# Kernel optimization log

Hardware: AMD Instinct MI355X
Metric: run time of the kernel (lower is better)

The kernel has to match this reference:

```python
import jax, jax.numpy as jnp
import numpy as np

EPS = 1e-07

def setup_inputs() -> dict:
    key = jax.random.key(0)
    k1, k2, k3, k4 = jax.random.split(key, 4)
    B, IN, OUT = 8192, 2048, 2048
    input_tensor = jax.random.normal(k1, (B, IN), dtype=jnp.float32)
    # truncated_normal(stddev=0.02) init approximated with scaled normal
    W_hat = 0.02 * jax.random.normal(k2, (IN, OUT), dtype=jnp.float32)
    M_hat = 0.02 * jax.random.normal(k3, (IN, OUT), dtype=jnp.float32)
    gate = 0.02 * jax.random.normal(k4, (IN, OUT), dtype=jnp.float32)
    return {"input_tensor": input_tensor, "W_hat": W_hat, "M_hat": M_hat, "gate": gate}

def reference(input_tensor, W_hat, M_hat, gate):
    W = jnp.tanh(W_hat) * jax.nn.sigmoid(M_hat)          # [IN, OUT]
    a = input_tensor @ W                                  # additive path [B, OUT]
    m = jnp.exp(jnp.log(jnp.abs(input_tensor) + EPS) @ W) # multiplicative path [B, OUT]
    g = jax.nn.sigmoid(input_tensor @ gate)               # gate [B, OUT]
    return g * a + (1.0 - g) * m
```

## Files before the change

### kernel.cpp

```cpp
#include <hip/hip_runtime.h>
#include <stdint.h>

typedef __attribute__((ext_vector_type(8))) short short8;
typedef __attribute__((ext_vector_type(4))) float floatx4;

#define B_DIM 8192
#define K_DIM 2048
#define N_DIM 2048

__device__ __forceinline__ unsigned short f2bf(float f) {
    union { float f; unsigned u; } v; v.f = f;
    unsigned r = v.u + 0x7fffu + ((v.u >> 16) & 1u);
    return (unsigned short)(r >> 16);
}

__device__ __forceinline__ void gld_lds16(const void* g, void* l) {
    __builtin_amdgcn_global_load_lds(
        (const __attribute__((address_space(1))) void*)g,
        (__attribute__((address_space(3))) void*)l, 16, 0, 0);
}

__global__ __launch_bounds__(256) void prep_x(const float4* __restrict__ X4,
                                              ushort* __restrict__ Xb,
                                              ushort* __restrict__ Lb) {
    int i = blockIdx.x * 256 + threadIdx.x;
    float4 v = X4[i];
    ushort4 xb, lb;
    xb.x = f2bf(v.x); xb.y = f2bf(v.y); xb.z = f2bf(v.z); xb.w = f2bf(v.w);
    lb.x = f2bf(__logf(fabsf(v.x) + 1e-7f));
    lb.y = f2bf(__logf(fabsf(v.y) + 1e-7f));
    lb.z = f2bf(__logf(fabsf(v.z) + 1e-7f));
    lb.w = f2bf(__logf(fabsf(v.w) + 1e-7f));
    *(ushort4*)(Xb + (size_t)i * 4) = xb;
    *(ushort4*)(Lb + (size_t)i * 4) = lb;
}

__global__ __launch_bounds__(256) void prep_wg(const float* __restrict__ Wh,
                                               const float* __restrict__ Mh,
                                               const float* __restrict__ Gf,
                                               ushort* __restrict__ Wt,
                                               ushort* __restrict__ Gt) {
    __shared__ float tw[32][33];
    __shared__ float tg[32][33];
    const int k0 = blockIdx.y * 32, n0 = blockIdx.x * 32;
    const int tx = threadIdx.x, ty = threadIdx.y;
#pragma unroll
    for (int i = 0; i < 4; i++) {
        int k = k0 + ty + i * 8;
        int n = n0 + tx;
        size_t idx = (size_t)k * N_DIM + n;
        float wh = Wh[idx], mh = Mh[idx];
        tw[ty + i * 8][tx] = tanhf(wh) * (1.f / (1.f + __expf(-mh)));
        tg[ty + i * 8][tx] = Gf[idx];
    }
    __syncthreads();
#pragma unroll
    for (int i = 0; i < 4; i++) {
        int n = n0 + ty + i * 8;
        int k = k0 + tx;
        Wt[(size_t)n * K_DIM + k] = f2bf(tw[tx][ty + i * 8]);
        Gt[(size_t)n * K_DIM + k] = f2bf(tg[tx][ty + i * 8]);
    }
}

__global__ __launch_bounds__(256, 2) void gemm_fused(const ushort* __restrict__ Xb,
                                                     const ushort* __restrict__ Lb,
                                                     const ushort* __restrict__ Wt,
                                                     const ushort* __restrict__ Gt,
                                                     float* __restrict__ out) {
    __shared__ ushort smem[4 * 128 * 32];
    ushort* sX = smem;
    ushort* sL = smem + 1 * 128 * 32;
    ushort* sW = smem + 2 * 128 * 32;
    ushort* sG = smem + 3 * 128 * 32;

    const int t = threadIdx.x;
    const int lane = t & 63;
    const int w = t >> 6;
    const int wm = w >> 1, wn = w & 1;
    const int rowA = blockIdx.y * 128;
    const int rowB = blockIdx.x * 128;

    floatx4 acca[4][4], accm[4][4], accg[4][4];
    const floatx4 z = {0.f, 0.f, 0.f, 0.f};
#pragma unroll
    for (int i = 0; i < 4; i++)
#pragma unroll
        for (int j = 0; j < 4; j++) { acca[i][j] = z; accm[i][j] = z; accg[i][j] = z; }

    const int r0 = t >> 2;
    const int c8 = (t & 3) << 3;
    const int aoff0 = (rowA + r0) * K_DIM + c8;
    const int aoff1 = aoff0 + 64 * K_DIM;
    const int boff0 = (rowB + r0) * K_DIM + c8;
    const int boff1 = boff0 + 64 * K_DIM;

    const int lr = lane & 15;
    const int lk = (lane >> 4) << 3;
    const ushort* rdA = sX + (wm * 64 + lr) * 32 + lk;
    const ushort* rdB = sW + (wn * 64 + lr) * 32 + lk;

    for (int k0 = 0; k0 < K_DIM; k0 += 32) {
        gld_lds16(Xb + aoff0 + k0, sX + t * 8);
        gld_lds16(Xb + aoff1 + k0, sX + (t + 256) * 8);
        gld_lds16(Lb + aoff0 + k0, sL + t * 8);
        gld_lds16(Lb + aoff1 + k0, sL + (t + 256) * 8);
        gld_lds16(Wt + boff0 + k0, sW + t * 8);
        gld_lds16(Wt + boff1 + k0, sW + (t + 256) * 8);
        gld_lds16(Gt + boff0 + k0, sG + t * 8);
        gld_lds16(Gt + boff1 + k0, sG + (t + 256) * 8);
        asm volatile("s_waitcnt vmcnt(0)" ::: "memory");
        __syncthreads();
        short8 bw[4], bg[4];
#pragma unroll
        for (int ni = 0; ni < 4; ni++) {
            bw[ni] = *(const short8*)(rdB + ni * 16 * 32);
            bg[ni] = *(const short8*)(rdB + (128 * 32) + ni * 16 * 32);
        }
#pragma unroll
        for (int mi = 0; mi < 4; mi++) {
            short8 ax = *(const short8*)(rdA + mi * 16 * 32);
            short8 al = *(const short8*)(rdA + (128 * 32) + mi * 16 * 32);
#pragma unroll
            for (int ni = 0; ni < 4; ni++) {
                acca[mi][ni] = __builtin_amdgcn_mfma_f32_16x16x32_bf16(ax, bw[ni], acca[mi][ni], 0, 0, 0);
                accm[mi][ni] = __builtin_amdgcn_mfma_f32_16x16x32_bf16(al, bw[ni], accm[mi][ni], 0, 0, 0);
                accg[mi][ni] = __builtin_amdgcn_mfma_f32_16x16x32_bf16(ax, bg[ni], accg[mi][ni], 0, 0, 0);
            }
        }
        __syncthreads();
    }

    const int rsub = (lane >> 4) << 2;
#pragma unroll
    for (int mi = 0; mi < 4; mi++)
#pragma unroll
        for (int ni = 0; ni < 4; ni++)
#pragma unroll
            for (int r = 0; r < 4; r++) {
                int row = rowA + wm * 64 + mi * 16 + rsub + r;
                int col = rowB + wn * 64 + ni * 16 + lr;
                float g = 1.f / (1.f + __expf(-accg[mi][ni][r]));
                float a = acca[mi][ni][r];
                float m = __expf(accm[mi][ni][r]);
                out[(size_t)row * N_DIM + col] = g * a + (1.f - g) * m;
            }
}

extern "C" void kernel_launch(void* const* d_in, const int* in_sizes, int n_in,
                              void* d_out, int out_size, void* d_ws, size_t ws_size,
                              hipStream_t stream) {
    const float* X  = (const float*)d_in[0];
    const float* Wh = (const float*)d_in[1];
    const float* Mh = (const float*)d_in[2];
    const float* Gf = (const float*)d_in[3];
    float* out = (float*)d_out;

    char* ws = (char*)d_ws;
    ushort* Xb = (ushort*)(ws);
    ushort* Lb = (ushort*)(ws + (size_t)B_DIM * K_DIM * 2);
    ushort* Wt = (ushort*)(ws + (size_t)B_DIM * K_DIM * 4);
    ushort* Gt = (ushort*)(ws + (size_t)B_DIM * K_DIM * 4 + (size_t)N_DIM * K_DIM * 2);

    prep_x<<<dim3((B_DIM * K_DIM) / (256 * 4)), dim3(256), 0, stream>>>(
        (const float4*)X, Xb, Lb);

    prep_wg<<<dim3(N_DIM / 32, K_DIM / 32), dim3(32, 8), 0, stream>>>(Wh, Mh, Gf, Wt, Gt);

    gemm_fused<<<dim3(N_DIM / 128, B_DIM / 128), dim3(256), 0, stream>>>(Xb, Lb, Wt, Gt, out);
}
```

Baseline: 359.2 us.

## Swizzle GEMM LDS tiles with XOR and merge prep kernels into one launch

Adds an XOR swizzle to the 16-byte chunk positions of the GEMM's shared-memory tiles. Each thread fetches a permuted global column chunk, and the MFMA fragment reads apply the same permutation, so ds_read_b128 accesses avoid bank conflicts. The two preprocessing kernels become one launch: X-conversion blocks each handle two float4s, and weight blocks transpose 64x64 tiles with float4 loads and 16-byte stores. This is meant to cut LDS stalls in the main loop and launch and uncoalesced-store overhead in prep, at the cost of slightly more index arithmetic.

```diff
diff --git a/kernel.cpp b/kernel.cpp
--- a/kernel.cpp
+++ b/kernel.cpp
@@ -7,12 +7,17 @@
 #define B_DIM 8192
 #define K_DIM 2048
 #define N_DIM 2048
+#define PREP_X_BLOCKS 8192
 
 __device__ __forceinline__ unsigned short f2bf(float f) {
     union { float f; unsigned u; } v; v.f = f;
     unsigned r = v.u + 0x7fffu + ((v.u >> 16) & 1u);
     return (unsigned short)(r >> 16);
 }
+__device__ __forceinline__ unsigned pack2bf(float a, float b) {
+    return (unsigned)f2bf(a) | ((unsigned)f2bf(b) << 16);
+}
+__device__ __forceinline__ float sigm(float x) { return 1.f / (1.f + __expf(-x)); }
 
 __device__ __forceinline__ void gld_lds16(const void* g, void* l) {
     __builtin_amdgcn_global_load_lds(
@@ -20,47 +25,71 @@
         (__attribute__((address_space(3))) void*)l, 16, 0, 0);
 }
 
-__global__ __launch_bounds__(256) void prep_x(const float4* __restrict__ X4,
-                                              ushort* __restrict__ Xb,
-                                              ushort* __restrict__ Lb) {
-    int i = blockIdx.x * 256 + threadIdx.x;
-    float4 v = X4[i];
-    ushort4 xb, lb;
-    xb.x = f2bf(v.x); xb.y = f2bf(v.y); xb.z = f2bf(v.z); xb.w = f2bf(v.w);
-    lb.x = f2bf(__logf(fabsf(v.x) + 1e-7f));
-    lb.y = f2bf(__logf(fabsf(v.y) + 1e-7f));
-    lb.z = f2bf(__logf(fabsf(v.z) + 1e-7f));
-    lb.w = f2bf(__logf(fabsf(v.w) + 1e-7f));
-    *(ushort4*)(Xb + (size_t)i * 4) = xb;
-    *(ushort4*)(Lb + (size_t)i * 4) = lb;
-}
-
-__global__ __launch_bounds__(256) void prep_wg(const float* __restrict__ Wh,
-                                               const float* __restrict__ Mh,
-                                               const float* __restrict__ Gf,
-                                               ushort* __restrict__ Wt,
-                                               ushort* __restrict__ Gt) {
-    __shared__ float tw[32][33];
-    __shared__ float tg[32][33];
-    const int k0 = blockIdx.y * 32, n0 = blockIdx.x * 32;
-    const int tx = threadIdx.x, ty = threadIdx.y;
+__global__ __launch_bounds__(256) void prep_all(const float4* __restrict__ X4,
+                                                ushort* __restrict__ Xb,
+                                                ushort* __restrict__ Lb,
+                                                const float* __restrict__ Wh,
+                                                const float* __restrict__ Mh,
+                                                const float* __restrict__ Gf,
+                                                ushort* __restrict__ Wt,
+                                                ushort* __restrict__ Gt) {
+    __shared__ ushort sw[64 * 66];
+    __shared__ ushort sg[64 * 66];
+    const int t = threadIdx.x;
+    int bid = blockIdx.x;
+    if (bid < PREP_X_BLOCKS) {
+        size_t i = (size_t)bid * 512 + t;
 #pragma unroll
-    for (int i = 0; i < 4; i++) {
-        int k = k0 + ty + i * 8;
-        int n = n0 + tx;
-        size_t idx = (size_t)k * N_DIM + n;
-        float wh = Wh[idx], mh = Mh[idx];
-        tw[ty + i * 8][tx] = tanhf(wh) * (1.f / (1.f + __expf(-mh)));
-        tg[ty + i * 8][tx] = Gf[idx];
+        for (int h = 0; h < 2; h++) {
+            float4 v = X4[i + h * 256];
+            ushort4 xb, lb;
+            xb.x = f2bf(v.x); xb.y = f2bf(v.y); xb.z = f2bf(v.z); xb.w = f2bf(v.w);
+            lb.x = f2bf(__logf(fabsf(v.x) + 1e-7f));
+            lb.y = f2bf(__logf(fabsf(v.y) + 1e-7f));
+            lb.z = f2bf(__logf(fabsf(v.z) + 1e-7f));
+            lb.w = f2bf(__logf(fabsf(v.w) + 1e-7f));
+            *(ushort4*)(Xb + (i + h * 256) * 4) = xb;
+            *(ushort4*)(Lb + (i + h * 256) * 4) = lb;
+        }
+        return;
+    }
+    bid -= PREP_X_BLOCKS;
+    const int n0 = (bid & 31) * 64;
+    const int k0 = (bid >> 5) * 64;
+    const int kr = t >> 4;
+    const int nc = (t & 15) * 4;
+#pragma unroll
+    for (int p = 0; p < 4; p++) {
+        const int kl = kr + p * 16;
+        const size_t idx = (size_t)(k0 + kl) * N_DIM + n0 + nc;
+        float4 wh = *(const float4*)(Wh + idx);
+        float4 mh = *(const float4*)(Mh + idx);
+        float4 gf = *(const float4*)(Gf + idx);
+        const int la = kl * 66 + nc;
+        *(unsigned*)(sw + la)     = pack2bf(tanhf(wh.x) * sigm(mh.x), tanhf(wh.y) * sigm(mh.y));
+        *(unsigned*)(sw + la + 2) = pack2bf(tanhf(wh.z) * sigm(mh.z), tanhf(wh.w) * sigm(mh.w));
+        *(unsigned*)(sg + la)     = pack2bf(gf.x, gf.y);
+        *(unsigned*)(sg + la + 2) = pack2bf(gf.z, gf.w);
     }
     __syncthreads();
+    const int nl = t >> 2;
+    const int kg = t & 3;
+    ushort tw[16], tg[16];
 #pragma unroll
-    for (int i = 0; i < 4; i++) {
-        int n = n0 + ty + i * 8;
-        int k = k0 + tx;
-        Wt[(size_t)n * K_DIM + k] = f2bf(tw[tx][ty + i * 8]);
-        Gt[(size_t)n * K_DIM + k] = f2bf(tg[tx][ty + i * 8]);
+    for (int j = 0; j < 16; j++) {
+        const int k = kg * 16 + j;
+        tw[j] = sw[k * 66 + nl];
+        tg[j] = sg[k * 66 + nl];
     }
+    const size_t o = (size_t)(n0 + nl) * K_DIM + k0 + kg * 16;
+    short8 vw0 = {(short)tw[0],(short)tw[1],(short)tw[2],(short)tw[3],(short)tw[4],(short)tw[5],(short)tw[6],(short)tw[7]};
+    short8 vw1 = {(short)tw[8],(short)tw[9],(short)tw[10],(short)tw[11],(short)tw[12],(short)tw[13],(short)tw[14],(short)tw[15]};
+    short8 vg0 = {(short)tg[0],(short)tg[1],(short)tg[2],(short)tg[3],(short)tg[4],(short)tg[5],(short)tg[6],(short)tg[7]};
+    short8 vg1 = {(short)tg[8],(short)tg[9],(short)tg[10],(short)tg[11],(short)tg[12],(short)tg[13],(short)tg[14],(short)tg[15]};
+    *(short8*)(Wt + o) = vw0;
+    *(short8*)(Wt + o + 8) = vw1;
+    *(short8*)(Gt + o) = vg0;
+    *(short8*)(Gt + o + 8) = vg1;
 }
 
 __global__ __launch_bounds__(256, 2) void gemm_fused(const ushort* __restrict__ Xb,
@@ -89,16 +118,16 @@
         for (int j = 0; j < 4; j++) { acca[i][j] = z; accm[i][j] = z; accg[i][j] = z; }
 
     const int r0 = t >> 2;
-    const int c8 = (t & 3) << 3;
-    const int aoff0 = (rowA + r0) * K_DIM + c8;
+    const int cs = (((t & 3) ^ ((t >> 3) & 3)) << 3);
+    const int aoff0 = (rowA + r0) * K_DIM + cs;
     const int aoff1 = aoff0 + 64 * K_DIM;
-    const int boff0 = (rowB + r0) * K_DIM + c8;
+    const int boff0 = (rowB + r0) * K_DIM + cs;
     const int boff1 = boff0 + 64 * K_DIM;
 
     const int lr = lane & 15;
-    const int lk = (lane >> 4) << 3;
-    const ushort* rdA = sX + (wm * 64 + lr) * 32 + lk;
-    const ushort* rdB = sW + (wn * 64 + lr) * 32 + lk;
+    const int xorc = (((lane >> 4) ^ ((lr >> 1) & 3)) << 3);
+    const ushort* rdA = sX + (wm * 64 + lr) * 32 + xorc;
+    const ushort* rdB = sW + (wn * 64 + lr) * 32 + xorc;
 
     for (int k0 = 0; k0 < K_DIM; k0 += 32) {
         gld_lds16(Xb + aoff0 + k0, sX + t * 8);
@@ -140,7 +169,7 @@
             for (int r = 0; r < 4; r++) {
                 int row = rowA + wm * 64 + mi * 16 + rsub + r;
                 int col = rowB + wn * 64 + ni * 16 + lr;
-                float g = 1.f / (1.f + __expf(-accg[mi][ni][r]));
+                float g = sigm(accg[mi][ni][r]);
                 float a = acca[mi][ni][r];
                 float m = __expf(accm[mi][ni][r]);
                 out[(size_t)row * N_DIM + col] = g * a + (1.f - g) * m;
@@ -162,10 +191,8 @@
     ushort* Wt = (ushort*)(ws + (size_t)B_DIM * K_DIM * 4);
     ushort* Gt = (ushort*)(ws + (size_t)B_DIM * K_DIM * 4 + (size_t)N_DIM * K_DIM * 2);
 
-    prep_x<<<dim3((B_DIM * K_DIM) / (256 * 4)), dim3(256), 0, stream>>>(
-        (const float4*)X, Xb, Lb);
-
-    prep_wg<<<dim3(N_DIM / 32, K_DIM / 32), dim3(32, 8), 0, stream>>>(Wh, Mh, Gf, Wt, Gt);
+    prep_all<<<dim3(PREP_X_BLOCKS + (N_DIM / 64) * (K_DIM / 64)), dim3(256), 0, stream>>>(
+        (const float4*)X, Xb, Lb, Wh, Mh, Gf, Wt, Gt);
 
     gemm_fused<<<dim3(N_DIM / 128, B_DIM / 128), dim3(256), 0, stream>>>(Xb, Lb, Wt, Gt, out);
 }
```

New measurement: 362.7 us. No clear change (+1.0%).
